# Optimization experiments

Measured on AMD Instinct MI355X. Metric: run time of the kernel, lower is better.

The kernel has to match this reference:

```python
import jax, jax.numpy as jnp
import numpy as np

DISTANCE_WEIGHT = 1.001  # self.distence_weight in the torch module


def setup_inputs() -> dict:
    key = jax.random.key(0)
    k1, k2 = jax.random.split(key)
    B, DIM_IN, DIM_OUT = 1024, 512, 512
    x = jax.random.normal(k1, (B, DIM_IN), dtype=jnp.float32)
    centers = jax.random.normal(k2, (DIM_OUT, DIM_IN), dtype=jnp.float32)
    beta = jnp.ones((DIM_OUT,), dtype=jnp.float32)
    return {"x": x, "centers": centers, "beta": beta}


def reference(x, centers, beta):
    # L1 pairwise distance: [B, dim_out]
    sim = jnp.sum(jnp.abs(x[:, None, :] - centers[None, :, :]), axis=-1)
    # negate, shift by global max * distance_weight, scale by beta
    sim = -sim + jnp.max(sim) * DISTANCE_WEIGHT
    return beta * sim
```

## Files before the change

kernel.cpp:

```cpp
#include <hip/hip_runtime.h>


typedef _Float16 h2 __attribute__((ext_vector_type(2)));
typedef float f4 __attribute__((ext_vector_type(4)));
typedef unsigned int u32x4 __attribute__((ext_vector_type(4)));
typedef unsigned int u32x2 __attribute__((ext_vector_type(2)));

#define DIM_B 1024
#define DIM_O 512
#define DIM_K 512
#define BM 32
#define BN 64
#define BK 64
#define KH (BK / 2)
#define W_DIST 1.001f

__device__ __forceinline__ h2 as_h2(unsigned int u) { h2 r; __builtin_memcpy(&r, &u, 4); return r; }
__device__ __forceinline__ unsigned int as_u(h2 h) { unsigned int r; __builtin_memcpy(&r, &h, 4); return r; }

__global__ __launch_bounds__(256) void k_sim(const float* __restrict__ X,
                                             const float* __restrict__ C,
                                             float* __restrict__ S,
                                             float* __restrict__ bmax)
{
    __shared__ __align__(16) h2 xs[KH][BM];
    __shared__ __align__(16) h2 cs[KH][BN];
    const int tid = threadIdx.x;
    const int bx = blockIdx.x & 7;
    const int by = blockIdx.x >> 3;
    const int row0 = by * BM, col0 = bx * BN;
    const int tr = tid >> 5;
    const int tc = tid & 31;
    float acc[4][2] = {};
    const h2 one2 = {(_Float16)1.f, (_Float16)1.f};

    for (int k0 = 0; k0 < DIM_K; k0 += BK) {
#pragma unroll
        for (int p = 0; p < 2; ++p) {
            int s = tid + p * 256;
            int row = s >> 4, kv = s & 15;
            f4 v = *(const f4*)(X + (row0 + row) * DIM_K + k0 + kv * 4);
            int ka = 2 * kv, kb = ka + 1;
            h2 h0 = {(_Float16)v.x, (_Float16)v.y};
            h2 h1 = {(_Float16)v.z, (_Float16)v.w};
            xs[ka][row ^ ((ka & 7) << 2)] = h0;
            xs[kb][row ^ ((kb & 7) << 2)] = h1;
        }
#pragma unroll
        for (int p = 0; p < 4; ++p) {
            int s = tid + p * 256;
            int row = s >> 4, kv = s & 15;
            f4 v = *(const f4*)(C + (col0 + row) * DIM_K + k0 + kv * 4);
            int ka = 2 * kv, kb = ka + 1;
            h2 h0 = {(_Float16)v.x, (_Float16)v.y};
            h2 h1 = {(_Float16)v.z, (_Float16)v.w};
            cs[ka][row ^ ((ka & 7) << 2)] = h0;
            cs[kb][row ^ ((kb & 7) << 2)] = h1;
        }
        __syncthreads();
#pragma unroll
        for (int k2 = 0; k2 < KH; ++k2) {
            const int sw = k2 & 7;
            u32x4 xu = *(const u32x4*)&xs[k2][4 * (tr ^ sw)];
            u32x2 cu = *(const u32x2*)&cs[k2][2 * (tc ^ (sw << 1))];
#pragma unroll
            for (int i = 0; i < 4; ++i) {
                h2 a = as_h2(xu[i]);
#pragma unroll
                for (int j = 0; j < 2; ++j) {
                    h2 d = a - as_h2(cu[j]);
                    h2 ad = as_h2(as_u(d) & 0x7fff7fffu);
                    acc[i][j] = __builtin_amdgcn_fdot2(ad, one2, acc[i][j], false);
                }
            }
        }
        __syncthreads();
    }

    const int r0 = row0 + tr * 4;
    const int c0 = col0 + tc * 2;
    float m = 0.f;
#pragma unroll
    for (int i = 0; i < 4; ++i) {
        float2 v = make_float2(acc[i][0], acc[i][1]);
        *(float2*)(S + (r0 + i) * DIM_O + c0) = v;
        m = fmaxf(m, fmaxf(v.x, v.y));
    }
#pragma unroll
    for (int off = 32; off > 0; off >>= 1)
        m = fmaxf(m, __shfl_xor(m, off, 64));
    __shared__ float wm[4];
    if ((tid & 63) == 0) wm[tid >> 6] = m;
    __syncthreads();
    if (tid == 0)
        bmax[blockIdx.x] = fmaxf(fmaxf(wm[0], wm[1]), fmaxf(wm[2], wm[3]));
}

__global__ __launch_bounds__(256) void k_out(float* __restrict__ S,
                                             const float* __restrict__ beta,
                                             const float* __restrict__ bmax)
{
    const int tid = threadIdx.x;
    const int lane = tid & 63;
    float m = fmaxf(fmaxf(bmax[lane], bmax[lane + 64]),
                    fmaxf(bmax[lane + 128], bmax[lane + 192]));
#pragma unroll
    for (int off = 32; off > 0; off >>= 1)
        m = fmaxf(m, __shfl_xor(m, off, 64));
    const float shift = m * W_DIST;

    const int f = blockIdx.x * 256 + tid;
    f4 s = ((const f4*)S)[f];
    f4 b = ((const f4*)beta)[f & 127];
    f4 r;
    r.x = b.x * (shift - s.x);
    r.y = b.y * (shift - s.y);
    r.z = b.z * (shift - s.z);
    r.w = b.w * (shift - s.w);
    ((f4*)S)[f] = r;
}

extern "C" void kernel_launch(void* const* d_in, const int* in_sizes, int n_in,
                              void* d_out, int out_size, void* d_ws, size_t ws_size,
                              hipStream_t stream) {
    const float* X = (const float*)d_in[0];
    const float* C = (const float*)d_in[1];
    const float* beta = (const float*)d_in[2];
    float* S = (float*)d_out;
    float* bmax = (float*)d_ws;
    k_sim<<<256, 256, 0, stream>>>(X, C, S, bmax);
    k_out<<<512, 256, 0, stream>>>(S, beta, bmax);
}
```

Baseline: 96.38 us.

## Use small single-wave tiles with register prefetch of next K slice

Shrinks the tile to 16x32 outputs per 64-thread block, launching 1024 blocks, so more blocks run across the GPU's compute units. Global loads for the next K slice are issued into registers before computing on the current slice, overlapping memory latency with the L1-distance math. Shared memory switches to a row-major padded layout with 128-bit LDS reads, and conversion uses packed cvt_pkrtz. Trade-offs: smaller tiles reuse each loaded element across fewer outputs and need more registers for prefetch, and k_out now reduces 1024 partial maxima.

```diff
diff --git a/kernel.cpp b/kernel.cpp
--- a/kernel.cpp
+++ b/kernel.cpp
@@ -6,94 +6,104 @@
 typedef unsigned int u32x4 __attribute__((ext_vector_type(4)));
 typedef unsigned int u32x2 __attribute__((ext_vector_type(2)));
 
-#define DIM_B 1024
 #define DIM_O 512
 #define DIM_K 512
-#define BM 32
-#define BN 64
+#define BM 16
+#define BN 32
 #define BK 64
-#define KH (BK / 2)
+#define LSTRIDE 36
 #define W_DIST 1.001f
 
-__device__ __forceinline__ h2 as_h2(unsigned int u) { h2 r; __builtin_memcpy(&r, &u, 4); return r; }
-__device__ __forceinline__ unsigned int as_u(h2 h) { unsigned int r; __builtin_memcpy(&r, &h, 4); return r; }
+__device__ __forceinline__ h2 as_h2(unsigned int u){ h2 r; __builtin_memcpy(&r,&u,4); return r; }
+__device__ __forceinline__ unsigned int as_u(h2 h){ unsigned int r; __builtin_memcpy(&r,&h,4); return r; }
+__device__ __forceinline__ unsigned int cvt2(float a, float b){
+    auto h = __builtin_amdgcn_cvt_pkrtz(a, b);
+    unsigned int r; __builtin_memcpy(&r, &h, 4); return r;
+}
 
-__global__ __launch_bounds__(256) void k_sim(const float* __restrict__ X,
-                                             const float* __restrict__ C,
-                                             float* __restrict__ S,
-                                             float* __restrict__ bmax)
+__global__ __launch_bounds__(64) void k_sim(const float* __restrict__ X,
+                                            const float* __restrict__ C,
+                                            float* __restrict__ S,
+                                            float* __restrict__ bmax)
 {
-    __shared__ __align__(16) h2 xs[KH][BM];
-    __shared__ __align__(16) h2 cs[KH][BN];
+    __shared__ __align__(16) h2 xs[BM][LSTRIDE];
+    __shared__ __align__(16) h2 cs[BN][LSTRIDE];
     const int tid = threadIdx.x;
-    const int bx = blockIdx.x & 7;
-    const int by = blockIdx.x >> 3;
+    const int bx = blockIdx.x & 15;
+    const int by = blockIdx.x >> 4;
     const int row0 = by * BM, col0 = bx * BN;
-    const int tr = tid >> 5;
-    const int tc = tid & 31;
+    const int tr = tid >> 4;
+    const int tc = tid & 15;
     float acc[4][2] = {};
     const h2 one2 = {(_Float16)1.f, (_Float16)1.f};
 
-    for (int k0 = 0; k0 < DIM_K; k0 += BK) {
+    f4 xv[4], cv[8];
+    const int srow = tid >> 4, skv = tid & 15;
 #pragma unroll
-        for (int p = 0; p < 2; ++p) {
-            int s = tid + p * 256;
-            int row = s >> 4, kv = s & 15;
-            f4 v = *(const f4*)(X + (row0 + row) * DIM_K + k0 + kv * 4);
-            int ka = 2 * kv, kb = ka + 1;
-            h2 h0 = {(_Float16)v.x, (_Float16)v.y};
-            h2 h1 = {(_Float16)v.z, (_Float16)v.w};
-            xs[ka][row ^ ((ka & 7) << 2)] = h0;
-            xs[kb][row ^ ((kb & 7) << 2)] = h1;
+    for (int p = 0; p < 4; ++p)
+        xv[p] = *(const f4*)(X + (row0 + srow + 4 * p) * DIM_K + 4 * skv);
+#pragma unroll
+    for (int p = 0; p < 8; ++p)
+        cv[p] = *(const f4*)(C + (col0 + srow + 4 * p) * DIM_K + 4 * skv);
+
+    for (int t = 0; t < 8; ++t) {
+        __syncthreads();
+#pragma unroll
+        for (int p = 0; p < 4; ++p) {
+            u32x2 w; w[0] = cvt2(xv[p].x, xv[p].y); w[1] = cvt2(xv[p].z, xv[p].w);
+            *(u32x2*)&xs[srow + 4 * p][skv * 2] = w;
         }
 #pragma unroll
-        for (int p = 0; p < 4; ++p) {
-            int s = tid + p * 256;
-            int row = s >> 4, kv = s & 15;
-            f4 v = *(const f4*)(C + (col0 + row) * DIM_K + k0 + kv * 4);
-            int ka = 2 * kv, kb = ka + 1;
-            h2 h0 = {(_Float16)v.x, (_Float16)v.y};
-            h2 h1 = {(_Float16)v.z, (_Float16)v.w};
-            cs[ka][row ^ ((ka & 7) << 2)] = h0;
-            cs[kb][row ^ ((kb & 7) << 2)] = h1;
+        for (int p = 0; p < 8; ++p) {
+            u32x2 w; w[0] = cvt2(cv[p].x, cv[p].y); w[1] = cvt2(cv[p].z, cv[p].w);
+            *(u32x2*)&cs[srow + 4 * p][skv * 2] = w;
         }
         __syncthreads();
+
+        const int kn = (t < 7) ? (t + 1) * BK : 0;
 #pragma unroll
-        for (int k2 = 0; k2 < KH; ++k2) {
-            const int sw = k2 & 7;
-            u32x4 xu = *(const u32x4*)&xs[k2][4 * (tr ^ sw)];
-            u32x2 cu = *(const u32x2*)&cs[k2][2 * (tc ^ (sw << 1))];
+        for (int p = 0; p < 4; ++p)
+            xv[p] = *(const f4*)(X + (row0 + srow + 4 * p) * DIM_K + kn + 4 * skv);
 #pragma unroll
-            for (int i = 0; i < 4; ++i) {
-                h2 a = as_h2(xu[i]);
+        for (int p = 0; p < 8; ++p)
+            cv[p] = *(const f4*)(C + (col0 + srow + 4 * p) * DIM_K + kn + 4 * skv);
+
 #pragma unroll
-                for (int j = 0; j < 2; ++j) {
-                    h2 d = a - as_h2(cu[j]);
-                    h2 ad = as_h2(as_u(d) & 0x7fff7fffu);
-                    acc[i][j] = __builtin_amdgcn_fdot2(ad, one2, acc[i][j], false);
+        for (int g = 0; g < 8; ++g) {
+            u32x4 xr[4], cr[2];
+#pragma unroll
+            for (int i = 0; i < 4; ++i)
+                xr[i] = *(const u32x4*)&xs[tr * 4 + i][g * 4];
+            cr[0] = *(const u32x4*)&cs[tc][g * 4];
+            cr[1] = *(const u32x4*)&cs[tc + 16][g * 4];
+#pragma unroll
+            for (int k2 = 0; k2 < 4; ++k2) {
+#pragma unroll
+                for (int i = 0; i < 4; ++i) {
+                    h2 a = as_h2(xr[i][k2]);
+#pragma unroll
+                    for (int j = 0; j < 2; ++j) {
+                        h2 d = a - as_h2(cr[j][k2]);
+                        h2 ad = as_h2(as_u(d) & 0x7fff7fffu);
+                        acc[i][j] = __builtin_amdgcn_fdot2(ad, one2, acc[i][j], false);
+                    }
                 }
             }
         }
-        __syncthreads();
     }
 
-    const int r0 = row0 + tr * 4;
-    const int c0 = col0 + tc * 2;
     float m = 0.f;
 #pragma unroll
     for (int i = 0; i < 4; ++i) {
-        float2 v = make_float2(acc[i][0], acc[i][1]);
-        *(float2*)(S + (r0 + i) * DIM_O + c0) = v;
-        m = fmaxf(m, fmaxf(v.x, v.y));
+        const int r = row0 + tr * 4 + i;
+        S[r * DIM_O + col0 + tc]      = acc[i][0];
+        S[r * DIM_O + col0 + tc + 16] = acc[i][1];
+        m = fmaxf(m, fmaxf(acc[i][0], acc[i][1]));
     }
 #pragma unroll
     for (int off = 32; off > 0; off >>= 1)
         m = fmaxf(m, __shfl_xor(m, off, 64));
-    __shared__ float wm[4];
-    if ((tid & 63) == 0) wm[tid >> 6] = m;
-    __syncthreads();
-    if (tid == 0)
-        bmax[blockIdx.x] = fmaxf(fmaxf(wm[0], wm[1]), fmaxf(wm[2], wm[3]));
+    if (tid == 0) bmax[blockIdx.x] = m;
 }
 
 __global__ __launch_bounds__(256) void k_out(float* __restrict__ S,
@@ -102,8 +112,10 @@
 {
     const int tid = threadIdx.x;
     const int lane = tid & 63;
-    float m = fmaxf(fmaxf(bmax[lane], bmax[lane + 64]),
-                    fmaxf(bmax[lane + 128], bmax[lane + 192]));
+    float m = 0.f;
+#pragma unroll
+    for (int i = 0; i < 16; ++i)
+        m = fmaxf(m, bmax[lane + 64 * i]);
 #pragma unroll
     for (int off = 32; off > 0; off >>= 1)
         m = fmaxf(m, __shfl_xor(m, off, 64));
@@ -128,6 +140,6 @@
     const float* beta = (const float*)d_in[2];
     float* S = (float*)d_out;
     float* bmax = (float*)d_ws;
-    k_sim<<<256, 256, 0, stream>>>(X, C, S, bmax);
+    k_sim<<<1024, 64, 0, stream>>>(X, C, S, bmax);
     k_out<<<512, 256, 0, stream>>>(S, beta, bmax);
 }
```

Result: faster. 79.58 us (-17.4%).
